# Optimization experiments

Measured on AMD Instinct MI355X. Metric: run time of the kernel, lower is better.

Reference implementation:

```python
import jax, jax.numpy as jnp
import numpy as np

B = 4194304  # batch of affine parameter vectors


def setup_inputs() -> dict:
    key = jax.random.key(0)
    vector = jax.random.normal(key, (B, 6), dtype=jnp.float32)
    return {"vector": vector}


def reference(vector):
    # vector: [B, 6] = (tx, ty, tz, angle_x, angle_y, angle_z)
    t = vector[:, :3]                      # [B, 3] translation
    ax, ay, az = vector[:, 3], vector[:, 4], vector[:, 5]

    cx, sx = jnp.cos(ax), jnp.sin(ax)
    cy, sy = jnp.cos(ay), jnp.sin(ay)
    cz, sz = jnp.cos(az), jnp.sin(az)
    one = jnp.ones_like(cx)
    zero = jnp.zeros_like(cx)

    # Batched 3x3 rotation matrices, rows stacked then columns: [B, 3, 3]
    x_rot = jnp.stack([
        jnp.stack([one, zero, zero], -1),
        jnp.stack([zero, cx, -sx], -1),
        jnp.stack([zero, sx, cx], -1),
    ], axis=-2)
    y_rot = jnp.stack([
        jnp.stack([cy, zero, sy], -1),
        jnp.stack([zero, one, zero], -1),
        jnp.stack([-sy, zero, cy], -1),
    ], axis=-2)
    z_rot = jnp.stack([
        jnp.stack([cz, -sz, zero], -1),
        jnp.stack([sz, cz, zero], -1),
        jnp.stack([zero, zero, one], -1),
    ], axis=-2)

    m_rot = jnp.einsum('bij,bjk,bkl->bil', x_rot, y_rot, z_rot)
    m_rot = m_rot - jnp.eye(3, dtype=vector.dtype)  # subtract identity (voxelmorph shift convention)

    matrix = jnp.concatenate([m_rot, t[:, :, None]], axis=2)  # [B, 3, 4]
    return matrix.reshape(vector.shape[0], 12)
```

## Files before the change

### kernel.cpp

```cpp
#include <hip/hip_runtime.h>


#define BLOCK 256
#define RPB   512

__global__ __launch_bounds__(BLOCK) void affine_to_matrix_staged(
    const float* __restrict__ in, float* __restrict__ out) {
    __shared__ float s_in[RPB * 6];
    __shared__ float s_out[RPB * 12];

    const int tid = threadIdx.x;
    const size_t rowBase = (size_t)blockIdx.x * RPB;
    const float4* gin  = reinterpret_cast<const float4*>(in  + rowBase * 6);
    float4*       gout = reinterpret_cast<float4*>(out + rowBase * 12);

    float4* s_in4 = reinterpret_cast<float4*>(s_in);
    #pragma unroll
    for (int k = 0; k < 3; ++k) {
        int g = tid + k * BLOCK;
        s_in4[g] = gin[g];
    }
    __syncthreads();

    const float4* myin = reinterpret_cast<const float4*>(s_in + tid * 12);
    float4 a = myin[0], b = myin[1], c = myin[2];
    float r[12] = {a.x, a.y, a.z, a.w, b.x, b.y, b.z, b.w, c.x, c.y, c.z, c.w};
    float4* myout = reinterpret_cast<float4*>(s_out + tid * 24);
    #pragma unroll
    for (int k2 = 0; k2 < 2; ++k2) {
        const float* v = r + k2 * 6;
        float sx, cx, sy, cy, sz, cz;
        __sincosf(v[3], &sx, &cx);
        __sincosf(v[4], &sy, &cy);
        __sincosf(v[5], &sz, &cz);
        float sxsy = sx * sy;
        float cxsy = cx * sy;
        float m0 = cy * cz - 1.0f, m1 = -cy * sz,               m2  = sy;
        float m4 = cx * sz + sxsy * cz, m5 = cx * cz - sxsy * sz - 1.0f, m6 = -sx * cy;
        float m8 = sx * sz - cxsy * cz, m9 = sx * cz + cxsy * sz, m10 = cx * cy - 1.0f;
        myout[k2 * 3 + 0] = make_float4(m0, m1, m2,  v[0]);
        myout[k2 * 3 + 1] = make_float4(m4, m5, m6,  v[1]);
        myout[k2 * 3 + 2] = make_float4(m8, m9, m10, v[2]);
    }
    __syncthreads();

    const float4* s_out4 = reinterpret_cast<const float4*>(s_out);
    #pragma unroll
    for (int k = 0; k < 6; ++k) {
        int g = tid + k * BLOCK;
        gout[g] = s_out4[g];
    }
}

__global__ __launch_bounds__(BLOCK) void affine_to_matrix_tail(
    const float* __restrict__ in, float* __restrict__ out,
    size_t rowStart, size_t nRows) {
    size_t i = rowStart + blockIdx.x * (size_t)BLOCK + threadIdx.x;
    if (i >= nRows) return;
    const float* v = in + i * 6;
    float tx = v[0], ty = v[1], tz = v[2];
    float sx, cx, sy, cy, sz, cz;
    __sincosf(v[3], &sx, &cx);
    __sincosf(v[4], &sy, &cy);
    __sincosf(v[5], &sz, &cz);
    float sxsy = sx * sy, cxsy = cx * sy;
    float* m = out + i * 12;
    m[0] = cy * cz - 1.0f;  m[1] = -cy * sz;                m[2]  = sy;             m[3]  = tx;
    m[4] = cx * sz + sxsy * cz; m[5] = cx * cz - sxsy * sz - 1.0f; m[6] = -sx * cy;  m[7]  = ty;
    m[8] = sx * sz - cxsy * cz; m[9] = sx * cz + cxsy * sz; m[10] = cx * cy - 1.0f;  m[11] = tz;
}

extern "C" void kernel_launch(void* const* d_in, const int* in_sizes, int n_in,
                              void* d_out, int out_size, void* d_ws, size_t ws_size,
                              hipStream_t stream) {
    const float* in = (const float*)d_in[0];
    float* out = (float*)d_out;
    size_t rows = (size_t)in_sizes[0] / 6;
    size_t fullBlocks = rows / RPB;
    if (fullBlocks) {
        affine_to_matrix_staged<<<(unsigned)fullBlocks, BLOCK, 0, stream>>>(in, out);
    }
    size_t rem = rows - fullBlocks * RPB;
    if (rem) {
        unsigned tailGrid = (unsigned)((rem + BLOCK - 1) / BLOCK);
        affine_to_matrix_tail<<<tailGrid, BLOCK, 0, stream>>>(in, out, fullBlocks * RPB, rows);
    }
}
```

Before: 51.37 us.

## Share one swizzled LDS buffer and use nontemporal global loads and stores

The separate input and output shared buffers are merged into one f32x4 array, which needs an extra barrier before outputs overwrite the inputs. Output writes into LDS use an XOR swizzle on the float4 index to reduce bank conflicts from the stride-6 per-thread pattern. Global loads and stores become nontemporal to avoid polluting caches in this streaming kernel. The smaller LDS footprint may allow more blocks per CU, at the cost of one more synchronization.

```diff
diff --git a/kernel.cpp b/kernel.cpp
--- a/kernel.cpp
+++ b/kernel.cpp
@@ -4,28 +4,30 @@
 #define BLOCK 256
 #define RPB   512
 
+typedef float f32x4 __attribute__((ext_vector_type(4)));
+
+__device__ __forceinline__ int swz(int i) { return i ^ ((i >> 3) & 7); }
+
 __global__ __launch_bounds__(BLOCK) void affine_to_matrix_staged(
     const float* __restrict__ in, float* __restrict__ out) {
-    __shared__ float s_in[RPB * 6];
-    __shared__ float s_out[RPB * 12];
+    __shared__ f32x4 s[RPB * 3];
 
     const int tid = threadIdx.x;
     const size_t rowBase = (size_t)blockIdx.x * RPB;
-    const float4* gin  = reinterpret_cast<const float4*>(in  + rowBase * 6);
-    float4*       gout = reinterpret_cast<float4*>(out + rowBase * 12);
+    const f32x4* gin  = reinterpret_cast<const f32x4*>(in  + rowBase * 6);
+    f32x4*       gout = reinterpret_cast<f32x4*>(out + rowBase * 12);
 
-    float4* s_in4 = reinterpret_cast<float4*>(s_in);
     #pragma unroll
     for (int k = 0; k < 3; ++k) {
         int g = tid + k * BLOCK;
-        s_in4[g] = gin[g];
+        s[g] = __builtin_nontemporal_load(&gin[g]);
     }
     __syncthreads();
 
-    const float4* myin = reinterpret_cast<const float4*>(s_in + tid * 12);
-    float4 a = myin[0], b = myin[1], c = myin[2];
+    f32x4 a = s[tid * 3 + 0], b = s[tid * 3 + 1], c = s[tid * 3 + 2];
     float r[12] = {a.x, a.y, a.z, a.w, b.x, b.y, b.z, b.w, c.x, c.y, c.z, c.w};
-    float4* myout = reinterpret_cast<float4*>(s_out + tid * 24);
+    __syncthreads();
+
     #pragma unroll
     for (int k2 = 0; k2 < 2; ++k2) {
         const float* v = r + k2 * 6;
@@ -35,20 +37,20 @@
         __sincosf(v[5], &sz, &cz);
         float sxsy = sx * sy;
         float cxsy = cx * sy;
-        float m0 = cy * cz - 1.0f, m1 = -cy * sz,               m2  = sy;
-        float m4 = cx * sz + sxsy * cz, m5 = cx * cz - sxsy * sz - 1.0f, m6 = -sx * cy;
-        float m8 = sx * sz - cxsy * cz, m9 = sx * cz + cxsy * sz, m10 = cx * cy - 1.0f;
-        myout[k2 * 3 + 0] = make_float4(m0, m1, m2,  v[0]);
-        myout[k2 * 3 + 1] = make_float4(m4, m5, m6,  v[1]);
-        myout[k2 * 3 + 2] = make_float4(m8, m9, m10, v[2]);
+        int base = tid * 6 + k2 * 3;
+        f32x4 m0 = {cy * cz - 1.0f,      -cy * sz,                    sy,             v[0]};
+        f32x4 m1 = {cx * sz + sxsy * cz, cx * cz - sxsy * sz - 1.0f,  -sx * cy,       v[1]};
+        f32x4 m2 = {sx * sz - cxsy * cz, sx * cz + cxsy * sz,         cx * cy - 1.0f, v[2]};
+        s[swz(base + 0)] = m0;
+        s[swz(base + 1)] = m1;
+        s[swz(base + 2)] = m2;
     }
     __syncthreads();
 
-    const float4* s_out4 = reinterpret_cast<const float4*>(s_out);
     #pragma unroll
     for (int k = 0; k < 6; ++k) {
         int g = tid + k * BLOCK;
-        gout[g] = s_out4[g];
+        __builtin_nontemporal_store(s[swz(g)], &gout[g]);
     }
 }
 
@@ -58,16 +60,15 @@
     size_t i = rowStart + blockIdx.x * (size_t)BLOCK + threadIdx.x;
     if (i >= nRows) return;
     const float* v = in + i * 6;
-    float tx = v[0], ty = v[1], tz = v[2];
     float sx, cx, sy, cy, sz, cz;
     __sincosf(v[3], &sx, &cx);
     __sincosf(v[4], &sy, &cy);
     __sincosf(v[5], &sz, &cz);
     float sxsy = sx * sy, cxsy = cx * sy;
     float* m = out + i * 12;
-    m[0] = cy * cz - 1.0f;  m[1] = -cy * sz;                m[2]  = sy;             m[3]  = tx;
-    m[4] = cx * sz + sxsy * cz; m[5] = cx * cz - sxsy * sz - 1.0f; m[6] = -sx * cy;  m[7]  = ty;
-    m[8] = sx * sz - cxsy * cz; m[9] = sx * cz + cxsy * sz; m[10] = cx * cy - 1.0f;  m[11] = tz;
+    m[0] = cy * cz - 1.0f;      m[1] = -cy * sz;                   m[2]  = sy;              m[3]  = v[0];
+    m[4] = cx * sz + sxsy * cz; m[5] = cx * cz - sxsy * sz - 1.0f; m[6]  = -sx * cy;        m[7]  = v[1];
+    m[8] = sx * sz - cxsy * cz; m[9] = sx * cz + cxsy * sz;        m[10] = cx * cy - 1.0f;  m[11] = v[2];
 }
 
 extern "C" void kernel_launch(void* const* d_in, const int* in_sizes, int n_in,
```

Measured after the change: 56.50 us. 1.1x slower.
